# Kernel tuning notes

Hardware: AMD Instinct MI355X
Metric: run time of the kernel (lower is better)

Reference implementation:

```python
import jax, jax.numpy as jnp
import numpy as np

B, C, CI, H, W = 4, 256, 128, 64, 64  # batch, in_channels, inter_channels, spatial


def setup_inputs() -> dict:
    key = jax.random.key(0)
    ks = jax.random.split(key, 9)
    p = lambda k, shape: jax.random.normal(k, shape, jnp.float32) * 0.05
    return {
        "x": jax.random.normal(ks[0], (B, C, H, W), jnp.float32),
        "g_w": p(ks[1], (CI, C)), "g_b": p(ks[2], (CI,)),
        "theta_w": p(ks[3], (CI, C)), "theta_b": p(ks[4], (CI,)),
        "phi_w": p(ks[5], (CI, C)), "phi_b": p(ks[6], (CI,)),
        "out_w": p(ks[7], (C, CI)), "out_b": p(ks[8], (C,)),
    }


def reference(x, g_w, g_b, theta_w, theta_b, phi_w, phi_b, out_w, out_b):
    n, c, h, w = x.shape
    xf = x.reshape(n, c, h * w)  # (b, C, N)
    # 1x1 convs as channel matmuls
    g_x = jnp.einsum('bcn,oc->bno', xf, g_w) + g_b              # (b, N, CI)
    theta_x = jnp.einsum('bcn,oc->bno', xf, theta_w) + theta_b  # (b, N, CI)
    phi_x = jnp.einsum('bcn,oc->bon', xf, phi_w) + phi_b[:, None]  # (b, CI, N)
    # 'channel' whitening: theta centered over channel axis per position,
    # phi centered over spatial axis per channel (as in source)
    theta_x = theta_x - theta_x.mean(axis=2, keepdims=True)
    phi_x = phi_x - phi_x.mean(axis=2, keepdims=True)
    # no softmax / no scaling in this forward
    pairwise = jnp.einsum('bnc,bcm->bnm', theta_x, phi_x)  # (b, N, N)
    y = jnp.einsum('bnm,bmc->bnc', pairwise, g_x)          # (b, N, CI)
    out = jnp.einsum('bnc,oc->bon', y, out_w) + out_b[:, None]  # (b, C, N)
    return x + out.reshape(n, c, h, w)
```

## Files before the change

### kernel.cpp

```cpp
#include <hip/hip_runtime.h>

constexpr int kB  = 4;
constexpr int kC  = 256;
constexpr int kCI = 128;
constexpr int kN  = 64 * 64;


constexpr int kSplits = 16;
constexpr int kSliceN = kN / kSplits;

typedef __attribute__((ext_vector_type(8))) short bf16x8;
typedef __attribute__((ext_vector_type(4))) float f32x4;

__device__ inline ushort f2b(float f) {
    unsigned u = __float_as_uint(f);
    return (ushort)((u + 0x7FFF + ((u >> 16) & 1)) >> 16);
}
__device__ inline float b2f(ushort u) { return __uint_as_float((unsigned)u << 16); }

constexpr long kOffTwcT = 0;
constexpr long kOffTbc  = kOffTwcT + kC * kCI;
constexpr long kOffPG   = kOffTbc + kCI;
constexpr long kOffRs   = kOffPG + (long)kB * kC * kN / 2;
constexpr long kOffT    = kOffRs + kB * kC;
constexpr long kOffW2t  = kOffT + kB * kCI * kCI;
constexpr long kOffMtH  = kOffW2t + kB * kC * kCI;
constexpr long kOffBeta = kOffMtH + (long)kB * kC * kC / 2;
constexpr long kOffXT   = kOffBeta + kB * kC;

__global__ void __launch_bounds__(256, 4)
xt_fused(const float* __restrict__ x, ushort* __restrict__ xT,
         const float* __restrict__ theta_w, const float* __restrict__ theta_b,
         float* __restrict__ twcT, float* __restrict__ tbc,
         float* __restrict__ rs, float* __restrict__ T) {
    __shared__ __align__(16) float smem[128 * 65];
    int t = threadIdx.x;
    if (blockIdx.y == 4) {
        int idx = blockIdx.z * 64 + blockIdx.x;
        T[(long)idx * 256 + t] = 0.f;
        if (idx >= 4) return;
        __shared__ float part[64][4];
        __shared__ float meanv[64];
        __shared__ float smr[128];
        float (*Ls)[65] = (float(*)[65])smem;
        int blk = idx, c0 = blk * 64;
        rs[blk * 256 + t] = 0.f;
#pragma unroll
        for (int it = 0; it < 8; it++) {
            int l = t + 256 * it;
            int k = l >> 4, c4 = (l & 15) * 4;
            float4 v = *(const float4*)(theta_w + (long)k * kC + c0 + c4);
            Ls[k][c4 + 0] = v.x; Ls[k][c4 + 1] = v.y;
            Ls[k][c4 + 2] = v.z; Ls[k][c4 + 3] = v.w;
        }
        __syncthreads();
        {
            int c = t >> 2, q = t & 3;
            float s = 0.f;
#pragma unroll
            for (int k = 0; k < 32; k++) s += Ls[q * 32 + k][c];
            part[c][q] = s;
        }
        __syncthreads();
        if (t < 64)
            meanv[t] = (part[t][0] + part[t][1] + part[t][2] + part[t][3]) * (1.f / kCI);
        __syncthreads();
        {
            int c = t >> 2, ks = (t & 3) * 32;
            float* dst = twcT + (long)(c0 + c) * kCI + ks;
            float m = meanv[c];
#pragma unroll
            for (int k = 0; k < 32; k++) dst[k] = Ls[ks + k][c] - m;
        }
        if (blk == 0) {
            if (t < 128) smr[t] = theta_b[t];
            __syncthreads();
            for (int st = 64; st > 0; st >>= 1) {
                if (t < st) smr[t] += smr[t + st];
                __syncthreads();
            }
            float bmean = smr[0] * (1.f / kCI);
            if (t < 128) tbc[t] = theta_b[t] - bmean;
        }
        return;
    }
    int b = blockIdx.z;
    int n0 = blockIdx.x * 64, c0 = blockIdx.y * 64;
    float (*ft)[66] = (float(*)[66])smem;
    const float* xb = x + (long)b * kC * kN;
#pragma unroll
    for (int i = 0; i < 4; i++) {
        int l = t + 256 * i;
        int row = l >> 4, col4 = (l & 15) * 4;
        float4 v = *(const float4*)(xb + (long)(c0 + row) * kN + n0 + col4);
        ft[row][col4 + 0] = v.x; ft[row][col4 + 1] = v.y;
        ft[row][col4 + 2] = v.z; ft[row][col4 + 3] = v.w;
    }
    __syncthreads();
    {
        int n = t >> 2, cs = (t & 3) * 16;
        unsigned w[8];
#pragma unroll
        for (int j = 0; j < 8; j++) {
            ushort lo = f2b(ft[cs + 2 * j][n]);
            ushort hi = f2b(ft[cs + 2 * j + 1][n]);
            w[j] = (unsigned)lo | ((unsigned)hi << 16);
        }
        ushort* dst = xT + ((long)b * kN + n0 + n) * kC + c0 + cs;
        ((uint4*)dst)[0] = make_uint4(w[0], w[1], w[2], w[3]);
        ((uint4*)dst)[1] = make_uint4(w[4], w[5], w[6], w[7]);
    }
}

__global__ void __launch_bounds__(256, 2)
pg_mfma(const float* __restrict__ phi_w, const float* __restrict__ g_w,
        const ushort* __restrict__ xT, ushort* __restrict__ PGh,
        float* __restrict__ rs) {
    int b = blockIdx.z;
    int r0 = blockIdx.y * 128, n0 = blockIdx.x * 128;
    const float* wbase = blockIdx.y == 0 ? phi_w : g_w;
    __shared__ ushort Ws[128 * 40];
    __shared__ ushort Xs[128 * 40];
    int t = threadIdx.x;
    int w = t >> 6, lane = t & 63, q = lane >> 4, ln = lane & 15;
    f32x4 acc[2][8];
#pragma unroll
    for (int i = 0; i < 2; i++)
#pragma unroll
        for (int j = 0; j < 8; j++) acc[i][j] = 0.f;
    const ushort* xTb = xT + ((long)b * kN + n0) * kC;
    for (int kc = 0; kc < kC; kc += 32) {
        __syncthreads();
#pragma unroll
        for (int it = 0; it < 4; it++) {
            int l = t + 256 * it;
            int row = l >> 3, seg = l & 7;
            float4 v = *(const float4*)(wbase + (long)row * kC + kc + seg * 4);
            ushort4 u = {f2b(v.x), f2b(v.y), f2b(v.z), f2b(v.w)};
            *(ushort4*)&Ws[row * 40 + seg * 4] = u;
        }
#pragma unroll
        for (int it = 0; it < 2; it++) {
            int l = t + 256 * it;
            int row = l >> 2, seg = l & 3;
            uint4 v = *(const uint4*)(xTb + (long)row * kC + kc + seg * 8);
            *(uint4*)&Xs[row * 40 + seg * 8] = v;
        }
        __syncthreads();
        bf16x8 a[2], bb[8];
#pragma unroll
        for (int mt = 0; mt < 2; mt++)
            a[mt] = *(const bf16x8*)&Ws[(32 * w + 16 * mt + ln) * 40 + q * 8];
#pragma unroll
        for (int nt = 0; nt < 8; nt++)
            bb[nt] = *(const bf16x8*)&Xs[(16 * nt + ln) * 40 + q * 8];
#pragma unroll
        for (int mt = 0; mt < 2; mt++)
#pragma unroll
            for (int nt = 0; nt < 8; nt++)
                acc[mt][nt] = __builtin_amdgcn_mfma_f32_16x16x32_bf16(
                    a[mt], bb[nt], acc[mt][nt], 0, 0, 0);
    }
    ushort* pb = PGh + (long)b * kC * kN;
    float rpart[2][4] = {};
#pragma unroll
    for (int mt = 0; mt < 2; mt++)
#pragma unroll
        for (int nt = 0; nt < 8; nt++)
#pragma unroll
            for (int i = 0; i < 4; i++) {
                int row = r0 + 32 * w + 16 * mt + 4 * q + i;
                int col = n0 + 16 * nt + ln;
                ushort st = f2b(acc[mt][nt][i]);
                pb[(long)row * kN + col] = st;
                rpart[mt][i] += b2f(st);
            }
#pragma unroll
    for (int mt = 0; mt < 2; mt++)
#pragma unroll
        for (int i = 0; i < 4; i++) {
            float v = rpart[mt][i];
            v += __shfl_xor(v, 1);
            v += __shfl_xor(v, 2);
            v += __shfl_xor(v, 4);
            v += __shfl_xor(v, 8);
            if (ln == 0)
                atomicAdd(rs + b * kC + r0 + 32 * w + 16 * mt + 4 * q + i, v);
        }
}

__global__ void __launch_bounds__(256, 4)
tsplit_mfma(const ushort* __restrict__ PGh, float* __restrict__ T) {
    int s = blockIdx.x, b = blockIdx.z;
    int qy = blockIdx.y >> 1, qx = blockIdx.y & 1;
    long nbase = (long)s * kSliceN;
    __shared__ ushort As[64 * 40];
    __shared__ ushort Bs[64 * 40];
    int t = threadIdx.x;
    int w = t >> 6, lane = t & 63, q = lane >> 4, ln = lane & 15;
    f32x4 acc[4];
#pragma unroll
    for (int j = 0; j < 4; j++) acc[j] = 0.f;
    const ushort* Phi = PGh + ((long)b * kC + 64 * qy) * kN + nbase;
    const ushort* G2  = PGh + ((long)b * kC + kCI + 64 * qx) * kN + nbase;
    for (int kc = 0; kc < kSliceN; kc += 32) {
        __syncthreads();
        {
            int row = t >> 2, seg = t & 3;
            *(uint4*)&As[row * 40 + seg * 8] =
                *(const uint4*)(Phi + (long)row * kN + kc + seg * 8);
            *(uint4*)&Bs[row * 40 + seg * 8] =
                *(const uint4*)(G2 + (long)row * kN + kc + seg * 8);
        }
        __syncthreads();
        bf16x8 a = *(const bf16x8*)&As[(16 * w + ln) * 40 + q * 8];
#pragma unroll
        for (int nt = 0; nt < 4; nt++) {
            bf16x8 bb = *(const bf16x8*)&Bs[(16 * nt + ln) * 40 + q * 8];
            acc[nt] = __builtin_amdgcn_mfma_f32_16x16x32_bf16(a, bb, acc[nt], 0, 0, 0);
        }
    }
    float* Tb = T + (long)b * kCI * kCI;
#pragma unroll
    for (int nt = 0; nt < 4; nt++)
#pragma unroll
        for (int i = 0; i < 4; i++) {
            int c  = 64 * qy + 16 * w + 4 * q + i;
            int cp = 64 * qx + 16 * nt + ln;
            atomicAdd(&Tb[(long)c * kCI + cp], acc[nt][i]);
        }
}

__global__ void __launch_bounds__(256, 4)
w2t_kernel(const float* __restrict__ out_w, const float* __restrict__ T,
           const float* __restrict__ rs, float* __restrict__ W2t) {
    int b = blockIdx.z;
    const float* Tb = T + (long)b * kCI * kCI;
    float* Cb = W2t + (long)b * kC * kCI;
    __shared__ __align__(16) float As[16][68];
    __shared__ __align__(16) float Bs[16][68];
    int t = threadIdx.x;
    int tx = t & 15, ty = t >> 4;
    int m0 = blockIdx.y * 64, n0 = blockIdx.x * 64;
    float acc[4][4] = {};
    for (int kc = 0; kc < kCI; kc += 16) {
        __syncthreads();
        {
            int r = t >> 2, c4 = (t & 3) * 4;
            float4 va = *(const float4*)(out_w + (long)(m0 + r) * kCI + kc + c4);
            As[c4 + 0][r] = va.x; As[c4 + 1][r] = va.y;
            As[c4 + 2][r] = va.z; As[c4 + 3][r] = va.w;
            float4 vb = *(const float4*)(Tb + (long)(n0 + r) * kCI + kc + c4);
            float rp = rs[b * kC + n0 + r] * (1.f / kN);
            const float* rg = rs + b * kC + kCI + kc + c4;
            vb.x -= rp * rg[0]; vb.y -= rp * rg[1];
            vb.z -= rp * rg[2]; vb.w -= rp * rg[3];
            Bs[c4 + 0][r] = vb.x; Bs[c4 + 1][r] = vb.y;
            Bs[c4 + 2][r] = vb.z; Bs[c4 + 3][r] = vb.w;
        }
        __syncthreads();
#pragma unroll
        for (int k = 0; k < 16; k++) {
            float4 a = *(const float4*)&As[k][4 * ty];
            float4 bv = *(const float4*)&Bs[k][4 * tx];
            float av[4] = {a.x, a.y, a.z, a.w};
            float bw[4] = {bv.x, bv.y, bv.z, bv.w};
#pragma unroll
            for (int i = 0; i < 4; i++)
#pragma unroll
                for (int j = 0; j < 4; j++) acc[i][j] += av[i] * bw[j];
        }
    }
#pragma unroll
    for (int i = 0; i < 4; i++) {
        float4 ov = {acc[i][0], acc[i][1], acc[i][2], acc[i][3]};
        *(float4*)(Cb + (long)(m0 + 4 * ty + i) * kCI + n0 + 4 * tx) = ov;
    }
}

__global__ void __launch_bounds__(256, 4)
mt_kernel(const float* __restrict__ W2t, const float* __restrict__ twcT,
          const float* __restrict__ tbc, const float* __restrict__ out_b,
          ushort* __restrict__ Mth, float* __restrict__ beta) {
    int b = blockIdx.z;
    const float* Ab = W2t + (long)b * kC * kCI;
    ushort* Cb = Mth + (long)b * kC * kC;
    __shared__ __align__(16) float As[16][68];
    __shared__ __align__(16) float Bs[16][68];
    int t = threadIdx.x;
    int tx = t & 15, ty = t >> 4;
    int m0 = blockIdx.y * 64, n0 = blockIdx.x * 64;
    float acc[4][4] = {};
    float bacc = 0.f;
    for (int kc = 0; kc < kCI; kc += 16) {
        __syncthreads();
        {
            int r = t >> 2, c4 = (t & 3) * 4;
            float4 va = *(const float4*)(Ab + (long)(m0 + r) * kCI + kc + c4);
            As[c4 + 0][r] = va.x; As[c4 + 1][r] = va.y;
            As[c4 + 2][r] = va.z; As[c4 + 3][r] = va.w;
            float4 vb = *(const float4*)(twcT + (long)(n0 + r) * kCI + kc + c4);
            Bs[c4 + 0][r] = vb.x; Bs[c4 + 1][r] = vb.y;
            Bs[c4 + 2][r] = vb.z; Bs[c4 + 3][r] = vb.w;
        }
        __syncthreads();
        if (blockIdx.x == 0 && t < 64) {
#pragma unroll
            for (int k = 0; k < 16; k++) bacc += tbc[kc + k] * As[k][t];
        }
#pragma unroll
        for (int k = 0; k < 16; k++) {
            float4 a = *(const float4*)&As[k][4 * ty];
            float4 bv = *(const float4*)&Bs[k][4 * tx];
            float av[4] = {a.x, a.y, a.z, a.w};
            float bw[4] = {bv.x, bv.y, bv.z, bv.w};
#pragma unroll
            for (int i = 0; i < 4; i++)
#pragma unroll
                for (int j = 0; j < 4; j++) acc[i][j] += av[i] * bw[j];
        }
    }
#pragma unroll
    for (int i = 0; i < 4; i++) {
        ushort4 u = {f2b(acc[i][0]), f2b(acc[i][1]), f2b(acc[i][2]), f2b(acc[i][3])};
        *(ushort4*)(Cb + (long)(m0 + 4 * ty + i) * kC + n0 + 4 * tx) = u;
    }
    if (blockIdx.x == 0 && t < 64)
        beta[b * kC + m0 + t] = out_b[m0 + t] + bacc;
}

__global__ void __launch_bounds__(256, 2)
final_mfma(const float* __restrict__ x, const ushort* __restrict__ Mth,
           const ushort* __restrict__ xT, const float* __restrict__ beta,
           float* __restrict__ out) {
    int b = blockIdx.z;
    int o0 = blockIdx.y * 128, n0 = blockIdx.x * 128;
    const ushort* Mbh = Mth + (long)b * kC * kC;
    __shared__ ushort Ws[128 * 40];
    __shared__ ushort Xs[128 * 40];
    int t = threadIdx.x;
    int w = t >> 6, lane = t & 63, q = lane >> 4, ln = lane & 15;
    f32x4 acc[2][8];
#pragma unroll
    for (int i = 0; i < 2; i++)
#pragma unroll
        for (int j = 0; j < 8; j++) acc[i][j] = 0.f;
    const ushort* xTb = xT + ((long)b * kN + n0) * kC;
    for (int kc = 0; kc < kC; kc += 32) {
        __syncthreads();
#pragma unroll
        for (int it = 0; it < 2; it++) {
            int l = t + 256 * it;
            int row = l >> 2, seg = l & 3;
            uint4 v = *(const uint4*)(Mbh + (long)(o0 + row) * kC + kc + seg * 8);
            *(uint4*)&Ws[row * 40 + seg * 8] = v;
        }
#pragma unroll
        for (int it = 0; it < 2; it++) {
            int l = t + 256 * it;
            int row = l >> 2, seg = l & 3;
            uint4 v = *(const uint4*)(xTb + (long)row * kC + kc + seg * 8);
            *(uint4*)&Xs[row * 40 + seg * 8] = v;
        }
        __syncthreads();
        bf16x8 a[2], bb[8];
#pragma unroll
        for (int mt = 0; mt < 2; mt++)
            a[mt] = *(const bf16x8*)&Ws[(32 * w + 16 * mt + ln) * 40 + q * 8];
#pragma unroll
        for (int nt = 0; nt < 8; nt++)
            bb[nt] = *(const bf16x8*)&Xs[(16 * nt + ln) * 40 + q * 8];
#pragma unroll
        for (int mt = 0; mt < 2; mt++)
#pragma unroll
            for (int nt = 0; nt < 8; nt++)
                acc[mt][nt] = __builtin_amdgcn_mfma_f32_16x16x32_bf16(
                    a[mt], bb[nt], acc[mt][nt], 0, 0, 0);
    }
    const float* xb = x + (long)b * kC * kN;
    float* ob = out + (long)b * kC * kN;
#pragma unroll
    for (int mt = 0; mt < 2; mt++)
#pragma unroll
        for (int nt = 0; nt < 8; nt++)
#pragma unroll
            for (int i = 0; i < 4; i++) {
                int row = o0 + 32 * w + 16 * mt + 4 * q + i;
                int col = n0 + 16 * nt + ln;
                long idx = (long)row * kN + col;
                ob[idx] = acc[mt][nt][i] + xb[idx] + beta[b * kC + row];
            }
}

extern "C" void kernel_launch(void* const* d_in, const int* in_sizes, int n_in,
                              void* d_out, int out_size, void* d_ws, size_t ws_size,
                              hipStream_t stream) {
    const float* x       = (const float*)d_in[0];
    const float* g_w     = (const float*)d_in[1];
    const float* theta_w = (const float*)d_in[3];
    const float* theta_b = (const float*)d_in[4];
    const float* phi_w   = (const float*)d_in[5];
    const float* out_w   = (const float*)d_in[7];
    const float* out_b   = (const float*)d_in[8];
    float* out = (float*)d_out;
    float* ws  = (float*)d_ws;

    float*  twcT = ws + kOffTwcT;
    float*  tbc  = ws + kOffTbc;
    ushort* PGh  = (ushort*)(ws + kOffPG);
    float*  rs   = ws + kOffRs;
    float*  T    = ws + kOffT;
    float*  W2t  = ws + kOffW2t;
    ushort* Mth  = (ushort*)(ws + kOffMtH);
    float*  beta = ws + kOffBeta;
    ushort* xT   = (ushort*)(ws + kOffXT);

    xt_fused<<<dim3(kN / 64, 5, kB), 256, 0, stream>>>(x, xT, theta_w, theta_b,
                                                       twcT, tbc, rs, T);
    pg_mfma<<<dim3(kN / 128, 2, kB), 256, 0, stream>>>(phi_w, g_w, xT, PGh, rs);
    tsplit_mfma<<<dim3(kSplits, 4, kB), 256, 0, stream>>>(PGh, T);
    w2t_kernel<<<dim3(2, 4, kB), 256, 0, stream>>>(out_w, T, rs, W2t);
    mt_kernel<<<dim3(4, 4, kB), 256, 0, stream>>>(W2t, twcT, tbc, out_b, Mth, beta);
    final_mfma<<<dim3(kN / 128, 2, kB), 256, 0, stream>>>(x, Mth, xT, beta, out);
}
```

Before: 139.0 us.

## Fuse phi/g projection with T accumulation and merge W2t/Mt kernels

The phi/g projection and the phi·gᵀ reduction now run in one kernel. Each block computes a 256x64 tile of projected features into shared memory and immediately accumulates its contribution to T with MFMA and atomics, so the full bf16 PG intermediate is never written to or reread from global memory. The phi/g weights are pre-converted to bf16 once, inside the first kernel. The two small fp32 GEMM kernels (W2t and Mt) are merged into one kernel that keeps W2t in shared memory, cutting the launch count from six to four. The costs are many more fp32 atomics into T (one set per 64-column slice instead of per 16 splits), higher LDS use that lowers occupancy, and redundant W2t recomputation across the column blocks of wm_kernel.

```diff
diff --git a/kernel.cpp b/kernel.cpp
--- a/kernel.cpp
+++ b/kernel.cpp
@@ -6,9 +6,6 @@
 constexpr int kN  = 64 * 64;
 
 
-constexpr int kSplits = 16;
-constexpr int kSliceN = kN / kSplits;
-
 typedef __attribute__((ext_vector_type(8))) short bf16x8;
 typedef __attribute__((ext_vector_type(4))) float f32x4;
 
@@ -20,24 +17,34 @@
 
 constexpr long kOffTwcT = 0;
 constexpr long kOffTbc  = kOffTwcT + kC * kCI;
-constexpr long kOffPG   = kOffTbc + kCI;
-constexpr long kOffRs   = kOffPG + (long)kB * kC * kN / 2;
+constexpr long kOffRs   = kOffTbc + kCI;
 constexpr long kOffT    = kOffRs + kB * kC;
-constexpr long kOffW2t  = kOffT + kB * kCI * kCI;
-constexpr long kOffMtH  = kOffW2t + kB * kC * kCI;
-constexpr long kOffBeta = kOffMtH + (long)kB * kC * kC / 2;
-constexpr long kOffXT   = kOffBeta + kB * kC;
+constexpr long kOffBeta = kOffT + kB * kCI * kCI;
+constexpr long kOffPGW  = kOffBeta + kB * kC;
+constexpr long kOffMtH  = kOffPGW + (long)kC * kC / 2;
+constexpr long kOffXT   = kOffMtH + (long)kB * kC * kC / 2;
 
 __global__ void __launch_bounds__(256, 4)
 xt_fused(const float* __restrict__ x, ushort* __restrict__ xT,
          const float* __restrict__ theta_w, const float* __restrict__ theta_b,
+         const float* __restrict__ phi_w, const float* __restrict__ g_w,
          float* __restrict__ twcT, float* __restrict__ tbc,
-         float* __restrict__ rs, float* __restrict__ T) {
+         float* __restrict__ rs, float* __restrict__ T,
+         ushort* __restrict__ PGWh) {
     __shared__ __align__(16) float smem[128 * 65];
     int t = threadIdx.x;
     if (blockIdx.y == 4) {
         int idx = blockIdx.z * 64 + blockIdx.x;
         T[(long)idx * 256 + t] = 0.f;
+        {
+            const float* src = idx < kCI ? phi_w + (long)idx * kC
+                                         : g_w + (long)(idx - kCI) * kC;
+            if (t < 64) {
+                float4 v = *(const float4*)(src + 4 * t);
+                ushort4 u = {f2b(v.x), f2b(v.y), f2b(v.z), f2b(v.w)};
+                *(ushort4*)(PGWh + (long)idx * kC + 4 * t) = u;
+            }
+        }
         if (idx >= 4) return;
         __shared__ float part[64][4];
         __shared__ float meanv[64];
@@ -113,70 +120,65 @@
 }
 
 __global__ void __launch_bounds__(256, 2)
-pg_mfma(const float* __restrict__ phi_w, const float* __restrict__ g_w,
-        const ushort* __restrict__ xT, ushort* __restrict__ PGh,
-        float* __restrict__ rs) {
+pgt_mfma(const ushort* __restrict__ PGWh, const ushort* __restrict__ xT,
+         float* __restrict__ rs, float* __restrict__ T) {
     int b = blockIdx.z;
-    int r0 = blockIdx.y * 128, n0 = blockIdx.x * 128;
-    const float* wbase = blockIdx.y == 0 ? phi_w : g_w;
-    __shared__ ushort Ws[128 * 40];
-    __shared__ ushort Xs[128 * 40];
+    int n0 = blockIdx.x * 64;
+    __shared__ ushort Ws[256 * 40];
+    __shared__ ushort Xs[64 * 40];
+    __shared__ ushort PGs[256 * 72];
     int t = threadIdx.x;
     int w = t >> 6, lane = t & 63, q = lane >> 4, ln = lane & 15;
-    f32x4 acc[2][8];
-#pragma unroll
-    for (int i = 0; i < 2; i++)
-#pragma unroll
-        for (int j = 0; j < 8; j++) acc[i][j] = 0.f;
+    f32x4 acc[4][4];
+#pragma unroll
+    for (int i = 0; i < 4; i++)
+#pragma unroll
+        for (int j = 0; j < 4; j++) acc[i][j] = 0.f;
     const ushort* xTb = xT + ((long)b * kN + n0) * kC;
     for (int kc = 0; kc < kC; kc += 32) {
         __syncthreads();
 #pragma unroll
         for (int it = 0; it < 4; it++) {
             int l = t + 256 * it;
-            int row = l >> 3, seg = l & 7;
-            float4 v = *(const float4*)(wbase + (long)row * kC + kc + seg * 4);
-            ushort4 u = {f2b(v.x), f2b(v.y), f2b(v.z), f2b(v.w)};
-            *(ushort4*)&Ws[row * 40 + seg * 4] = u;
-        }
-#pragma unroll
-        for (int it = 0; it < 2; it++) {
-            int l = t + 256 * it;
             int row = l >> 2, seg = l & 3;
-            uint4 v = *(const uint4*)(xTb + (long)row * kC + kc + seg * 8);
-            *(uint4*)&Xs[row * 40 + seg * 8] = v;
-        }
-        __syncthreads();
-        bf16x8 a[2], bb[8];
-#pragma unroll
-        for (int mt = 0; mt < 2; mt++)
-            a[mt] = *(const bf16x8*)&Ws[(32 * w + 16 * mt + ln) * 40 + q * 8];
-#pragma unroll
-        for (int nt = 0; nt < 8; nt++)
+            *(uint4*)&Ws[row * 40 + seg * 8] =
+                *(const uint4*)(PGWh + (long)row * kC + kc + seg * 8);
+        }
+        {
+            int row = t >> 2, seg = t & 3;
+            *(uint4*)&Xs[row * 40 + seg * 8] =
+                *(const uint4*)(xTb + (long)row * kC + kc + seg * 8);
+        }
+        __syncthreads();
+        bf16x8 a[4], bb[4];
+#pragma unroll
+        for (int mt = 0; mt < 4; mt++)
+            a[mt] = *(const bf16x8*)&Ws[(64 * w + 16 * mt + ln) * 40 + q * 8];
+#pragma unroll
+        for (int nt = 0; nt < 4; nt++)
             bb[nt] = *(const bf16x8*)&Xs[(16 * nt + ln) * 40 + q * 8];
 #pragma unroll
-        for (int mt = 0; mt < 2; mt++)
-#pragma unroll
-            for (int nt = 0; nt < 8; nt++)
+        for (int mt = 0; mt < 4; mt++)
+#pragma unroll
+            for (int nt = 0; nt < 4; nt++)
                 acc[mt][nt] = __builtin_amdgcn_mfma_f32_16x16x32_bf16(
                     a[mt], bb[nt], acc[mt][nt], 0, 0, 0);
     }
-    ushort* pb = PGh + (long)b * kC * kN;
-    float rpart[2][4] = {};
-#pragma unroll
-    for (int mt = 0; mt < 2; mt++)
-#pragma unroll
-        for (int nt = 0; nt < 8; nt++)
+    float rpart[4][4] = {};
+#pragma unroll
+    for (int mt = 0; mt < 4; mt++)
+#pragma unroll
+        for (int nt = 0; nt < 4; nt++)
 #pragma unroll
             for (int i = 0; i < 4; i++) {
-                int row = r0 + 32 * w + 16 * mt + 4 * q + i;
-                int col = n0 + 16 * nt + ln;
+                int row = 64 * w + 16 * mt + 4 * q + i;
+                int col = 16 * nt + ln;
                 ushort st = f2b(acc[mt][nt][i]);
-                pb[(long)row * kN + col] = st;
+                PGs[row * 72 + col] = st;
                 rpart[mt][i] += b2f(st);
             }
 #pragma unroll
-    for (int mt = 0; mt < 2; mt++)
+    for (int mt = 0; mt < 4; mt++)
 #pragma unroll
         for (int i = 0; i < 4; i++) {
             float v = rpart[mt][i];
@@ -185,74 +187,72 @@
             v += __shfl_xor(v, 4);
             v += __shfl_xor(v, 8);
             if (ln == 0)
-                atomicAdd(rs + b * kC + r0 + 32 * w + 16 * mt + 4 * q + i, v);
-        }
-}
-
-__global__ void __launch_bounds__(256, 4)
-tsplit_mfma(const ushort* __restrict__ PGh, float* __restrict__ T) {
-    int s = blockIdx.x, b = blockIdx.z;
-    int qy = blockIdx.y >> 1, qx = blockIdx.y & 1;
-    long nbase = (long)s * kSliceN;
-    __shared__ ushort As[64 * 40];
-    __shared__ ushort Bs[64 * 40];
+                atomicAdd(rs + b * kC + 64 * w + 16 * mt + 4 * q + i, v);
+        }
+    __syncthreads();
+    f32x4 acc2[2][8];
+#pragma unroll
+    for (int i = 0; i < 2; i++)
+#pragma unroll
+        for (int j = 0; j < 8; j++) acc2[i][j] = 0.f;
+#pragma unroll
+    for (int kk = 0; kk < 64; kk += 32) {
+        bf16x8 a2[2], b2[8];
+#pragma unroll
+        for (int mt = 0; mt < 2; mt++)
+            a2[mt] = *(const bf16x8*)&PGs[(32 * w + 16 * mt + ln) * 72 + kk + q * 8];
+#pragma unroll
+        for (int nt = 0; nt < 8; nt++)
+            b2[nt] = *(const bf16x8*)&PGs[(128 + 16 * nt + ln) * 72 + kk + q * 8];
+#pragma unroll
+        for (int mt = 0; mt < 2; mt++)
+#pragma unroll
+            for (int nt = 0; nt < 8; nt++)
+                acc2[mt][nt] = __builtin_amdgcn_mfma_f32_16x16x32_bf16(
+                    a2[mt], b2[nt], acc2[mt][nt], 0, 0, 0);
+    }
+    float* Tb = T + (long)b * kCI * kCI;
+#pragma unroll
+    for (int mt = 0; mt < 2; mt++)
+#pragma unroll
+        for (int nt = 0; nt < 8; nt++)
+#pragma unroll
+            for (int i = 0; i < 4; i++) {
+                int c  = 32 * w + 16 * mt + 4 * q + i;
+                int cp = 16 * nt + ln;
+                atomicAdd(&Tb[(long)c * kCI + cp], acc2[mt][nt][i]);
+            }
+}
+
+__global__ void __launch_bounds__(256, 2)
+wm_kernel(const float* __restrict__ out_w, const float* __restrict__ T,
+          const float* __restrict__ rs, const float* __restrict__ twcT,
+          const float* __restrict__ tbc, const float* __restrict__ out_b,
+          ushort* __restrict__ Mth, float* __restrict__ beta) {
+    int b = blockIdx.z;
+    int m0 = blockIdx.y * 64, n0 = blockIdx.x * 64;
+    const float* Tb = T + (long)b * kCI * kCI;
+    __shared__ __align__(16) float As[16][68];
+    __shared__ __align__(16) float Bs[16][132];
+    __shared__ __align__(16) float W2s[128][68];
     int t = threadIdx.x;
-    int w = t >> 6, lane = t & 63, q = lane >> 4, ln = lane & 15;
-    f32x4 acc[4];
-#pragma unroll
-    for (int j = 0; j < 4; j++) acc[j] = 0.f;
-    const ushort* Phi = PGh + ((long)b * kC + 64 * qy) * kN + nbase;
-    const ushort* G2  = PGh + ((long)b * kC + kCI + 64 * qx) * kN + nbase;
-    for (int kc = 0; kc < kSliceN; kc += 32) {
-        __syncthreads();
-        {
-            int row = t >> 2, seg = t & 3;
-            *(uint4*)&As[row * 40 + seg * 8] =
-                *(const uint4*)(Phi + (long)row * kN + kc + seg * 8);
-            *(uint4*)&Bs[row * 40 + seg * 8] =
-                *(const uint4*)(G2 + (long)row * kN + kc + seg * 8);
-        }
-        __syncthreads();
-        bf16x8 a = *(const bf16x8*)&As[(16 * w + ln) * 40 + q * 8];
-#pragma unroll
-        for (int nt = 0; nt < 4; nt++) {
-            bf16x8 bb = *(const bf16x8*)&Bs[(16 * nt + ln) * 40 + q * 8];
-            acc[nt] = __builtin_amdgcn_mfma_f32_16x16x32_bf16(a, bb, acc[nt], 0, 0, 0);
-        }
-    }
-    float* Tb = T + (long)b * kCI * kCI;
-#pragma unroll
-    for (int nt = 0; nt < 4; nt++)
-#pragma unroll
-        for (int i = 0; i < 4; i++) {
-            int c  = 64 * qy + 16 * w + 4 * q + i;
-            int cp = 64 * qx + 16 * nt + ln;
-            atomicAdd(&Tb[(long)c * kCI + cp], acc[nt][i]);
-        }
-}
-
-__global__ void __launch_bounds__(256, 4)
-w2t_kernel(const float* __restrict__ out_w, const float* __restrict__ T,
-           const float* __restrict__ rs, float* __restrict__ W2t) {
-    int b = blockIdx.z;
-    const float* Tb = T + (long)b * kCI * kCI;
-    float* Cb = W2t + (long)b * kC * kCI;
-    __shared__ __align__(16) float As[16][68];
-    __shared__ __align__(16) float Bs[16][68];
-    int t = threadIdx.x;
-    int tx = t & 15, ty = t >> 4;
-    int m0 = blockIdx.y * 64, n0 = blockIdx.x * 64;
-    float acc[4][4] = {};
-    for (int kc = 0; kc < kCI; kc += 16) {
+    int tr = t >> 4, tc = t & 15;
+    float accA[4][8] = {};
+    for (int c0 = 0; c0 < kCI; c0 += 16) {
         __syncthreads();
         {
             int r = t >> 2, c4 = (t & 3) * 4;
-            float4 va = *(const float4*)(out_w + (long)(m0 + r) * kCI + kc + c4);
+            float4 va = *(const float4*)(out_w + (long)(m0 + r) * kCI + c0 + c4);
             As[c4 + 0][r] = va.x; As[c4 + 1][r] = va.y;
             As[c4 + 2][r] = va.z; As[c4 + 3][r] = va.w;
-            float4 vb = *(const float4*)(Tb + (long)(n0 + r) * kCI + kc + c4);
-            float rp = rs[b * kC + n0 + r] * (1.f / kN);
-            const float* rg = rs + b * kC + kCI + kc + c4;
+        }
+#pragma unroll
+        for (int it = 0; it < 2; it++) {
+            int l = t + 256 * it;
+            int r = l >> 2, c4 = (l & 3) * 4;
+            float4 vb = *(const float4*)(Tb + (long)r * kCI + c0 + c4);
+            float rp = rs[b * kC + r] * (1.f / kN);
+            const float* rg = rs + b * kC + kCI + c0 + c4;
             vb.x -= rp * rg[0]; vb.y -= rp * rg[1];
             vb.z -= rp * rg[2]; vb.w -= rp * rg[3];
             Bs[c4 + 0][r] = vb.x; Bs[c4 + 1][r] = vb.y;
@@ -261,72 +261,58 @@
         __syncthreads();
 #pragma unroll
         for (int k = 0; k < 16; k++) {
-            float4 a = *(const float4*)&As[k][4 * ty];
-            float4 bv = *(const float4*)&Bs[k][4 * tx];
+            float4 a = *(const float4*)&As[k][4 * tr];
+            float4 b0 = *(const float4*)&Bs[k][8 * tc];
+            float4 b1 = *(const float4*)&Bs[k][8 * tc + 4];
+            float av[4] = {a.x, a.y, a.z, a.w};
+            float bw[8] = {b0.x, b0.y, b0.z, b0.w, b1.x, b1.y, b1.z, b1.w};
+#pragma unroll
+            for (int i = 0; i < 4; i++)
+#pragma unroll
+                for (int j = 0; j < 8; j++) accA[i][j] += av[i] * bw[j];
+        }
+    }
+    __syncthreads();
+#pragma unroll
+    for (int i = 0; i < 4; i++)
+#pragma unroll
+        for (int j = 0; j < 8; j++) W2s[8 * tc + j][4 * tr + i] = accA[i][j];
+    __syncthreads();
+    if (blockIdx.x == 0 && t < 64) {
+        float s = out_b[m0 + t];
+#pragma unroll 8
+        for (int j = 0; j < kCI; j++) s += tbc[j] * W2s[j][t];
+        beta[b * kC + m0 + t] = s;
+    }
+    int ty = t >> 4, tx = t & 15;
+    float accB[4][4] = {};
+    for (int j0 = 0; j0 < kCI; j0 += 16) {
+        __syncthreads();
+        {
+            int r = t >> 2, c4 = (t & 3) * 4;
+            float4 vb = *(const float4*)(twcT + (long)(n0 + r) * kCI + j0 + c4);
+            As[c4 + 0][r] = vb.x; As[c4 + 1][r] = vb.y;
+            As[c4 + 2][r] = vb.z; As[c4 + 3][r] = vb.w;
+        }
+        __syncthreads();
+#pragma unroll
+        for (int k = 0; k < 16; k++) {
+            float4 a = *(const float4*)&W2s[j0 + k][4 * ty];
+            float4 bv = *(const float4*)&As[k][4 * tx];
             float av[4] = {a.x, a.y, a.z, a.w};
             float bw[4] = {bv.x, bv.y, bv.z, bv.w};
 #pragma unroll
             for (int i = 0; i < 4; i++)
 #pragma unroll
-                for (int j = 0; j < 4; j++) acc[i][j] += av[i] * bw[j];
-        }
-    }
+                for (int j = 0; j < 4; j++) accB[i][j] += av[i] * bw[j];
+        }
+    }
+    ushort* Cb = Mth + (long)b * kC * kC;
 #pragma unroll
     for (int i = 0; i < 4; i++) {
-        float4 ov = {acc[i][0], acc[i][1], acc[i][2], acc[i][3]};
-        *(float4*)(Cb + (long)(m0 + 4 * ty + i) * kCI + n0 + 4 * tx) = ov;
-    }
-}
-
-__global__ void __launch_bounds__(256, 4)
-mt_kernel(const float* __restrict__ W2t, const float* __restrict__ twcT,
-          const float* __restrict__ tbc, const float* __restrict__ out_b,
-          ushort* __restrict__ Mth, float* __restrict__ beta) {
-    int b = blockIdx.z;
-    const float* Ab = W2t + (long)b * kC * kCI;
-    ushort* Cb = Mth + (long)b * kC * kC;
-    __shared__ __align__(16) float As[16][68];
-    __shared__ __align__(16) float Bs[16][68];
-    int t = threadIdx.x;
-    int tx = t & 15, ty = t >> 4;
-    int m0 = blockIdx.y * 64, n0 = blockIdx.x * 64;
-    float acc[4][4] = {};
-    float bacc = 0.f;
-    for (int kc = 0; kc < kCI; kc += 16) {
-        __syncthreads();
-        {
-            int r = t >> 2, c4 = (t & 3) * 4;
-            float4 va = *(const float4*)(Ab + (long)(m0 + r) * kCI + kc + c4);
-            As[c4 + 0][r] = va.x; As[c4 + 1][r] = va.y;
-            As[c4 + 2][r] = va.z; As[c4 + 3][r] = va.w;
-            float4 vb = *(const float4*)(twcT + (long)(n0 + r) * kCI + kc + c4);
-            Bs[c4 + 0][r] = vb.x; Bs[c4 + 1][r] = vb.y;
-            Bs[c4 + 2][r] = vb.z; Bs[c4 + 3][r] = vb.w;
-        }
-        __syncthreads();
-        if (blockIdx.x == 0 && t < 64) {
-#pragma unroll
-            for (int k = 0; k < 16; k++) bacc += tbc[kc + k] * As[k][t];
-        }
-#pragma unroll
-        for (int k = 0; k < 16; k++) {
-            float4 a = *(const float4*)&As[k][4 * ty];
-            float4 bv = *(const float4*)&Bs[k][4 * tx];
-            float av[4] = {a.x, a.y, a.z, a.w};
-            float bw[4] = {bv.x, bv.y, bv.z, bv.w};
-#pragma unroll
-            for (int i = 0; i < 4; i++)
-#pragma unroll
-                for (int j = 0; j < 4; j++) acc[i][j] += av[i] * bw[j];
-        }
-    }
-#pragma unroll
-    for (int i = 0; i < 4; i++) {
-        ushort4 u = {f2b(acc[i][0]), f2b(acc[i][1]), f2b(acc[i][2]), f2b(acc[i][3])};
+        ushort4 u = {f2b(accB[i][0]), f2b(accB[i][1]), f2b(accB[i][2]), f2b(accB[i][3])};
         *(ushort4*)(Cb + (long)(m0 + 4 * ty + i) * kC + n0 + 4 * tx) = u;
     }
-    if (blockIdx.x == 0 && t < 64)
-        beta[b * kC + m0 + t] = out_b[m0 + t] + bacc;
 }
 
 __global__ void __launch_bounds__(256, 2)
@@ -407,19 +393,17 @@
 
     float*  twcT = ws + kOffTwcT;
     float*  tbc  = ws + kOffTbc;
-    ushort* PGh  = (ushort*)(ws + kOffPG);
     float*  rs   = ws + kOffRs;
     float*  T    = ws + kOffT;
-    float*  W2t  = ws + kOffW2t;
+    float*  beta = ws + kOffBeta;
+    ushort* PGWh = (ushort*)(ws + kOffPGW);
     ushort* Mth  = (ushort*)(ws + kOffMtH);
-    float*  beta = ws + kOffBeta;
     ushort* xT   = (ushort*)(ws + kOffXT);
 
-    xt_fused<<<dim3(kN / 64, 5, kB), 256, 0, stream>>>(x, xT, theta_w, theta_b,
-                                                       twcT, tbc, rs, T);
-    pg_mfma<<<dim3(kN / 128, 2, kB), 256, 0, stream>>>(phi_w, g_w, xT, PGh, rs);
-    tsplit_mfma<<<dim3(kSplits, 4, kB), 256, 0, stream>>>(PGh, T);
-    w2t_kernel<<<dim3(2, 4, kB), 256, 0, stream>>>(out_w, T, rs, W2t);
-    mt_kernel<<<dim3(4, 4, kB), 256, 0, stream>>>(W2t, twcT, tbc, out_b, Mth, beta);
+    xt_fused<<<dim3(kN / 64, 5, kB), 256, 0, stream>>>(
+        x, xT, theta_w, theta_b, phi_w, g_w, twcT, tbc, rs, T, PGWh);
+    pgt_mfma<<<dim3(kN / 64, 1, kB), 256, 0, stream>>>(PGWh, xT, rs, T);
+    wm_kernel<<<dim3(4, 4, kB), 256, 0, stream>>>(out_w, T, rs, twcT, tbc,
+                                                  out_b, Mth, beta);
     final_mfma<<<dim3(kN / 128, 2, kB), 256, 0, stream>>>(x, Mth, xT, beta, out);
 }
```

After: 150.4 us. 1.08x slower.
